# Performance work log

Hardware: AMD Instinct MI355X
Metric: run time of the kernel (lower is better)

Reference implementation:

```python
import jax, jax.numpy as jnp
import numpy as np

B = 65536      # batch
HID = 128      # hidden_dim
Q = 4          # IRK stages
DT = 0.1       # default time step
N_ITERS = 10   # fixed-point iterations


def setup_inputs() -> dict:
    key = jax.random.key(0)
    ks = jax.random.split(key, 16)
    def lin(k, fan_in, fan_out):
        return jax.random.normal(k, (fan_in, fan_out), jnp.float32) / np.sqrt(fan_in)
    return {
        "X0": jax.random.normal(ks[0], (B, 4), jnp.float32),
        "W1": lin(ks[1], 4, HID),   "b1": jnp.zeros((HID,), jnp.float32),
        "W2": lin(ks[2], HID, HID), "b2": jnp.zeros((HID,), jnp.float32),
        "W3": lin(ks[3], HID, HID), "b3": jnp.zeros((HID,), jnp.float32),
        "W4": lin(ks[4], HID, 4),   "b4": jnp.zeros((4,), jnp.float32),
        "lam1": jax.random.normal(ks[5], (1,), jnp.float32) * 0.1 + 0.5,
        "lam2": jax.random.normal(ks[6], (1,), jnp.float32) * 0.1 + 0.5,
        "lam3": jax.random.normal(ks[7], (1,), jnp.float32) * 0.1 + 0.5,
        "lam4": jax.random.normal(ks[8], (1,), jnp.float32) * 0.1 + 0.5,
        "IRK_alpha": jax.random.normal(ks[9], (Q, Q), jnp.float32) * 0.25,
        "IRK_beta": jax.random.normal(ks[10], (Q,), jnp.float32) * 0.25,
    }


def reference(X0, W1, b1, W2, b2, W3, b3, W4, b4,
              lam1, lam2, lam3, lam4, IRK_alpha, IRK_beta):
    dt = DT

    def mlp(x):  # (N,4) -> (N,4)
        h = jnp.tanh(x @ W1 + b1)
        h = jnp.tanh(h @ W2 + b2)
        h = jnp.tanh(h @ W3 + b3)
        return h @ W4 + b4

    def hamiltonian_vf(x):  # x: (N,4) = [p1,p2,q1,q2]
        H_out = mlp(x)
        dp_dt = -lam1 * H_out[:, 2:] - lam2 * x[:, 2:]
        dq_dt = lam3 * H_out[:, :2] + lam4 * x[:, :2]
        return jnp.concatenate([dp_dt, dq_dt], axis=1)

    bsz = X0.shape[0]
    K = jnp.zeros((bsz, Q, 4), X0.dtype)
    for _ in range(N_ITERS):  # small fixed trip count, unrolled
        # same contraction as original torch einsum 'bqi,ij->bqj'
        X_stages = X0[:, None, :] + dt * jnp.einsum('bqi,ij->bqj', K, IRK_alpha)
        K = hamiltonian_vf(X_stages.reshape(-1, 4)).reshape(bsz, Q, 4)

    # intended IRK final combine: X1 = X0 + dt * sum_q beta_q K[:,q,:]
    X1 = X0 + dt * jnp.einsum('bqi,q->bi', K, IRK_beta)
    return X1
```

## Files before the change

### kernel.cpp

```cpp
#include <hip/hip_runtime.h>
#include <hip/hip_bf16.h>
#include <stdint.h>

#define HID   128
#define DT    0.1f
#define NITER 10
#define RT    64
#define NT    256
#define HSTR  136

typedef __attribute__((ext_vector_type(8))) short bf16x8;
typedef __attribute__((ext_vector_type(4))) float f32x4;
typedef __attribute__((ext_vector_type(2))) unsigned int u32x2;
typedef __attribute__((ext_vector_type(4))) unsigned int u32x4;

struct alignas(16) Smem {
    uint16_t hA[RT * HSTR];
    uint16_t hB[RT * HSTR];
    uint16_t xb[RT * 8];
    uint32_t w4f[4 * 64 * 4];
    float    b1[HID], b2[HID], b3[HID];
    float    kk[RT * 4];
};

__device__ __forceinline__ uint16_t f2bf(float f) {
    uint32_t u = __float_as_uint(f);
    return (uint16_t)((u + 0x7fffu + ((u >> 16) & 1u)) >> 16);
}

__device__ __forceinline__ uint32_t pk2(float a, float b) {
    __hip_bfloat162 h = __float22bfloat162_rn(float2{a, b});
    return *reinterpret_cast<uint32_t*>(&h);
}

__device__ __forceinline__ float tanh_fast(float x) {
    float e = __builtin_amdgcn_exp2f(x * 2.885390081777927f);
    return fmaf(-2.0f, __builtin_amdgcn_rcpf(e + 1.0f), 1.0f);
}

__device__ __forceinline__ void dense_mfma(
    const bf16x8 (&wf)[2][4], const float* __restrict__ bias,
    const uint16_t* __restrict__ src, uint16_t* __restrict__ dst,
    int w, int ln, int g)
{
    f32x4 acc[2][4];
    #pragma unroll
    for (int mt = 0; mt < 2; ++mt) {
        f32x4 bs = *(const f32x4*)&bias[w * 32 + mt * 16 + 4 * g];
        #pragma unroll
        for (int nt = 0; nt < 4; ++nt) acc[mt][nt] = bs;
    }
    #pragma unroll
    for (int kt = 0; kt < 4; ++kt) {
        bf16x8 bfr[4];
        #pragma unroll
        for (int nt = 0; nt < 4; ++nt)
            bfr[nt] = *(const bf16x8*)&src[(nt * 16 + ln) * HSTR + kt * 32 + 8 * g];
        #pragma unroll
        for (int mt = 0; mt < 2; ++mt)
            #pragma unroll
            for (int nt = 0; nt < 4; ++nt)
                acc[mt][nt] = __builtin_amdgcn_mfma_f32_16x16x32_bf16(wf[mt][kt], bfr[nt], acc[mt][nt], 0, 0, 0);
    }
    #pragma unroll
    for (int mt = 0; mt < 2; ++mt) {
        int hb = w * 32 + mt * 16 + 4 * g;
        #pragma unroll
        for (int nt = 0; nt < 4; ++nt) {
            int r = nt * 16 + ln;
            u32x2 p;
            p.x = pk2(tanh_fast(acc[mt][nt][0]), tanh_fast(acc[mt][nt][1]));
            p.y = pk2(tanh_fast(acc[mt][nt][2]), tanh_fast(acc[mt][nt][3]));
            *(u32x2*)&dst[r * HSTR + hb] = p;
        }
    }
}

__global__ __launch_bounds__(NT, 3) void pinn_irk_mfma(
    const float* __restrict__ x0g,
    const float* __restrict__ w1g, const float* __restrict__ b1g,
    const float* __restrict__ w2g, const float* __restrict__ b2g,
    const float* __restrict__ w3g, const float* __restrict__ b3g,
    const float* __restrict__ w4g, const float* __restrict__ b4g,
    const float* __restrict__ l1g, const float* __restrict__ l2g,
    const float* __restrict__ l3g, const float* __restrict__ l4g,
    const float* __restrict__ alg, const float* __restrict__ beg,
    float* __restrict__ outg)
{
    __shared__ Smem S;
    const int t    = threadIdx.x;
    const int blk  = blockIdx.x;
    const int lane = t & 63;
    const int w    = t >> 6;
    const int ln   = lane & 15;
    const int g    = lane >> 4;
    const bool owner = (g == 0);
    const int r_own  = w * 16 + ln;

    const float L0 = l1g[0], L1v = l2g[0], L2v = l3g[0], L3v = l4g[0];
    const float B40 = b4g[0], B41 = b4g[1], B42 = b4g[2], B43 = b4g[3];

    if (t < HID) { S.b1[t] = b1g[t]; S.b2[t] = b2g[t]; S.b3[t] = b3g[t]; }
    {
        int r = t >> 2, c = 4 + (t & 3);
        S.xb[r * 8 + c] = 0;
    }
    {
        int kt = t >> 6, l = t & 63;
        int lns = l & 15, gs = l >> 4;
        uint32_t f[4];
        #pragma unroll
        for (int jj = 0; jj < 4; ++jj) {
            int k0 = kt * 32 + 8 * gs + 2 * jj;
            uint32_t lo = (lns < 4) ? (uint32_t)f2bf(w4g[k0 * 4 + lns]) : 0u;
            uint32_t hi = (lns < 4) ? (uint32_t)f2bf(w4g[(k0 + 1) * 4 + lns]) : 0u;
            f[jj] = lo | (hi << 16);
        }
        *(u32x4*)&S.w4f[t * 4] = (u32x4){f[0], f[1], f[2], f[3]};
    }

    float X0r[4] = {0.f, 0.f, 0.f, 0.f};
    float Xr[4]  = {0.f, 0.f, 0.f, 0.f};
    if (owner) {
        const float* xp = x0g + (blk * (RT / 4) + (r_own >> 2)) * 4;
        #pragma unroll
        for (int c = 0; c < 4; ++c) { X0r[c] = xp[c]; Xr[c] = X0r[c]; }
        u32x2 p;
        p.x = pk2(Xr[0], Xr[1]);
        p.y = pk2(Xr[2], Xr[3]);
        *(u32x2*)&S.xb[r_own * 8] = p;
    }

    bf16x8 w1f[2], w2f[2][4], w3f[2][4];
    {
        const int mcol = w * 32 + ln;
        #pragma unroll
        for (int mt = 0; mt < 2; ++mt) {
            bf16x8 f1;
            #pragma unroll
            for (int j = 0; j < 8; ++j) {
                int k = 8 * g + j;
                float v = (k < 4) ? w1g[k * HID + mcol + mt * 16] : 0.0f;
                f1[j] = (short)f2bf(v);
            }
            w1f[mt] = f1;
            #pragma unroll
            for (int kt = 0; kt < 4; ++kt) {
                bf16x8 f2, f3;
                #pragma unroll
                for (int j = 0; j < 8; ++j) {
                    int k = kt * 32 + 8 * g + j;
                    f2[j] = (short)f2bf(w2g[k * HID + mcol + mt * 16]);
                    f3[j] = (short)f2bf(w3g[k * HID + mcol + mt * 16]);
                }
                w2f[mt][kt] = f2;
                w3f[mt][kt] = f3;
            }
        }
    }
    __syncthreads();

    #pragma unroll 1
    for (int it = 0; it < NITER; ++it) {
        {
            f32x4 acc[2][4];
            #pragma unroll
            for (int mt = 0; mt < 2; ++mt) {
                f32x4 bs = *(const f32x4*)&S.b1[w * 32 + mt * 16 + 4 * g];
                #pragma unroll
                for (int nt = 0; nt < 4; ++nt) acc[mt][nt] = bs;
            }
            bf16x8 bfr[4];
            #pragma unroll
            for (int nt = 0; nt < 4; ++nt) bfr[nt] = (bf16x8){0,0,0,0,0,0,0,0};
            if (g == 0) {
                #pragma unroll
                for (int nt = 0; nt < 4; ++nt)
                    bfr[nt] = *(const bf16x8*)&S.xb[(nt * 16 + ln) * 8];
            }
            #pragma unroll
            for (int mt = 0; mt < 2; ++mt)
                #pragma unroll
                for (int nt = 0; nt < 4; ++nt)
                    acc[mt][nt] = __builtin_amdgcn_mfma_f32_16x16x32_bf16(w1f[mt], bfr[nt], acc[mt][nt], 0, 0, 0);
            #pragma unroll
            for (int mt = 0; mt < 2; ++mt) {
                int hb = w * 32 + mt * 16 + 4 * g;
                #pragma unroll
                for (int nt = 0; nt < 4; ++nt) {
                    int r = nt * 16 + ln;
                    u32x2 p;
                    p.x = pk2(tanh_fast(acc[mt][nt][0]), tanh_fast(acc[mt][nt][1]));
                    p.y = pk2(tanh_fast(acc[mt][nt][2]), tanh_fast(acc[mt][nt][3]));
                    *(u32x2*)&S.hA[r * HSTR + hb] = p;
                }
            }
        }
        __syncthreads();

        dense_mfma(w2f, S.b2, S.hA, S.hB, w, ln, g);
        __syncthreads();

        dense_mfma(w3f, S.b3, S.hB, S.hA, w, ln, g);
        __syncthreads();

        {
            f32x4 acc = (f32x4){0.f, 0.f, 0.f, 0.f};
            #pragma unroll
            for (int kt = 0; kt < 4; ++kt) {
                bf16x8 wfr = *(const bf16x8*)&S.w4f[(kt * 64 + lane) * 4];
                bf16x8 bfr = *(const bf16x8*)&S.hA[r_own * HSTR + kt * 32 + 8 * g];
                acc = __builtin_amdgcn_mfma_f32_16x16x32_bf16(wfr, bfr, acc, 0, 0, 0);
            }
            if (owner) {
                float h0 = acc[0] + B40, h1 = acc[1] + B41;
                float h2 = acc[2] + B42, h3 = acc[3] + B43;
                float kv0 = -L0 * h2 - L1v * Xr[2];
                float kv1 = -L0 * h3 - L1v * Xr[3];
                float kv2 =  L2v * h0 + L3v * Xr[0];
                float kv3 =  L2v * h1 + L3v * Xr[1];
                *(f32x4*)&S.kk[r_own * 4] = (f32x4){kv0, kv1, kv2, kv3};
                #pragma unroll
                for (int c = 0; c < 4; ++c) {
                    float s = kv0 * alg[c] + kv1 * alg[4 + c]
                            + kv2 * alg[8 + c] + kv3 * alg[12 + c];
                    Xr[c] = fmaf(DT, s, X0r[c]);
                }
                u32x2 p;
                p.x = pk2(Xr[0], Xr[1]);
                p.y = pk2(Xr[2], Xr[3]);
                *(u32x2*)&S.xb[r_own * 8] = p;
            }
        }
        __syncthreads();
    }

    if (t < RT) {
        int bb = t >> 2, i = t & 3;
        float s = beg[0] * S.kk[(bb * 4 + 0) * 4 + i]
                + beg[1] * S.kk[(bb * 4 + 1) * 4 + i]
                + beg[2] * S.kk[(bb * 4 + 2) * 4 + i]
                + beg[3] * S.kk[(bb * 4 + 3) * 4 + i];
        int bglob = blk * (RT / 4) + bb;
        outg[bglob * 4 + i] = x0g[bglob * 4 + i] + DT * s;
    }
}

extern "C" void kernel_launch(void* const* d_in, const int* in_sizes, int n_in,
                              void* d_out, int out_size, void* d_ws, size_t ws_size,
                              hipStream_t stream) {
    (void)in_sizes; (void)n_in; (void)d_ws; (void)ws_size; (void)out_size;

    const int n_rows = 65536 * 4;
    dim3 grid(n_rows / RT);
    dim3 block(NT);

    pinn_irk_mfma<<<grid, block, 0, stream>>>(
        (const float*)d_in[0],
        (const float*)d_in[1],  (const float*)d_in[2],
        (const float*)d_in[3],  (const float*)d_in[4],
        (const float*)d_in[5],  (const float*)d_in[6],
        (const float*)d_in[7],  (const float*)d_in[8],
        (const float*)d_in[9],  (const float*)d_in[10],
        (const float*)d_in[11], (const float*)d_in[12],
        (const float*)d_in[13], (const float*)d_in[14],
        (float*)d_out);
}
```

Before: 407.3 us.

## Use rational tanh approximation, keep biases in registers, alias kk into hB

Replaces the exp2+rcp tanh with a clamped Padé rational polynomial evaluated on float2 pairs, which removes the transcendental exp per element and permits packed FMA. Biases are now loaded into registers instead of shared memory, and the K output buffer reuses the hB region. LDS use drops, and launch bounds are raised from 3 to 4 blocks per CU to increase occupancy. The risks are register spills under the tighter bound and a less exact tanh near the clamp at ±3.5.

```diff
diff --git a/kernel.cpp b/kernel.cpp
--- a/kernel.cpp
+++ b/kernel.cpp
@@ -11,6 +11,7 @@
 
 typedef __attribute__((ext_vector_type(8))) short bf16x8;
 typedef __attribute__((ext_vector_type(4))) float f32x4;
+typedef __attribute__((ext_vector_type(2))) float f32x2;
 typedef __attribute__((ext_vector_type(2))) unsigned int u32x2;
 typedef __attribute__((ext_vector_type(4))) unsigned int u32x4;
 
@@ -19,8 +20,6 @@
     uint16_t hB[RT * HSTR];
     uint16_t xb[RT * 8];
     uint32_t w4f[4 * 64 * 4];
-    float    b1[HID], b2[HID], b3[HID];
-    float    kk[RT * 4];
 };
 
 __device__ __forceinline__ uint16_t f2bf(float f) {
@@ -33,23 +32,36 @@
     return *reinterpret_cast<uint32_t*>(&h);
 }
 
-__device__ __forceinline__ float tanh_fast(float x) {
-    float e = __builtin_amdgcn_exp2f(x * 2.885390081777927f);
-    return fmaf(-2.0f, __builtin_amdgcn_rcpf(e + 1.0f), 1.0f);
+__device__ __forceinline__ uint32_t tanh2_bf16(float a, float b) {
+    f32x2 x;
+    x.x = __builtin_amdgcn_fmed3f(a, -3.5f, 3.5f);
+    x.y = __builtin_amdgcn_fmed3f(b, -3.5f, 3.5f);
+    f32x2 s = x * x;
+    f32x2 n = s + 378.0f;
+    n = n * s + 17325.0f;
+    n = n * s + 135135.0f;
+    n = n * x;
+    f32x2 d = s * 28.0f + 3150.0f;
+    d = d * s + 62370.0f;
+    d = d * s + 135135.0f;
+    f32x2 r;
+    r.x = __builtin_amdgcn_rcpf(d.x);
+    r.y = __builtin_amdgcn_rcpf(d.y);
+    f32x2 res = n * r;
+    __hip_bfloat162 h = __float22bfloat162_rn(float2{res.x, res.y});
+    return *reinterpret_cast<uint32_t*>(&h);
 }
 
 __device__ __forceinline__ void dense_mfma(
-    const bf16x8 (&wf)[2][4], const float* __restrict__ bias,
+    const bf16x8 (&wf)[2][4], const f32x4 (&bs)[2],
     const uint16_t* __restrict__ src, uint16_t* __restrict__ dst,
     int w, int ln, int g)
 {
     f32x4 acc[2][4];
     #pragma unroll
-    for (int mt = 0; mt < 2; ++mt) {
-        f32x4 bs = *(const f32x4*)&bias[w * 32 + mt * 16 + 4 * g];
-        #pragma unroll
-        for (int nt = 0; nt < 4; ++nt) acc[mt][nt] = bs;
-    }
+    for (int mt = 0; mt < 2; ++mt)
+        #pragma unroll
+        for (int nt = 0; nt < 4; ++nt) acc[mt][nt] = bs[mt];
     #pragma unroll
     for (int kt = 0; kt < 4; ++kt) {
         bf16x8 bfr[4];
@@ -69,14 +81,14 @@
         for (int nt = 0; nt < 4; ++nt) {
             int r = nt * 16 + ln;
             u32x2 p;
-            p.x = pk2(tanh_fast(acc[mt][nt][0]), tanh_fast(acc[mt][nt][1]));
-            p.y = pk2(tanh_fast(acc[mt][nt][2]), tanh_fast(acc[mt][nt][3]));
+            p.x = tanh2_bf16(acc[mt][nt][0], acc[mt][nt][1]);
+            p.y = tanh2_bf16(acc[mt][nt][2], acc[mt][nt][3]);
             *(u32x2*)&dst[r * HSTR + hb] = p;
         }
     }
 }
 
-__global__ __launch_bounds__(NT, 3) void pinn_irk_mfma(
+__global__ __launch_bounds__(NT, 4) void pinn_irk_mfma(
     const float* __restrict__ x0g,
     const float* __restrict__ w1g, const float* __restrict__ b1g,
     const float* __restrict__ w2g, const float* __restrict__ b2g,
@@ -88,6 +100,7 @@
     float* __restrict__ outg)
 {
     __shared__ Smem S;
+    float* kkp = reinterpret_cast<float*>(S.hB);
     const int t    = threadIdx.x;
     const int blk  = blockIdx.x;
     const int lane = t & 63;
@@ -100,7 +113,15 @@
     const float L0 = l1g[0], L1v = l2g[0], L2v = l3g[0], L3v = l4g[0];
     const float B40 = b4g[0], B41 = b4g[1], B42 = b4g[2], B43 = b4g[3];
 
-    if (t < HID) { S.b1[t] = b1g[t]; S.b2[t] = b2g[t]; S.b3[t] = b3g[t]; }
+    f32x4 b1f[2], b2f[2], b3f[2];
+    #pragma unroll
+    for (int mt = 0; mt < 2; ++mt) {
+        int hb = w * 32 + mt * 16 + 4 * g;
+        b1f[mt] = *(const f32x4*)&b1g[hb];
+        b2f[mt] = *(const f32x4*)&b2g[hb];
+        b3f[mt] = *(const f32x4*)&b3g[hb];
+    }
+
     {
         int r = t >> 2, c = 4 + (t & 3);
         S.xb[r * 8 + c] = 0;
@@ -165,11 +186,9 @@
         {
             f32x4 acc[2][4];
             #pragma unroll
-            for (int mt = 0; mt < 2; ++mt) {
-                f32x4 bs = *(const f32x4*)&S.b1[w * 32 + mt * 16 + 4 * g];
-                #pragma unroll
-                for (int nt = 0; nt < 4; ++nt) acc[mt][nt] = bs;
-            }
+            for (int mt = 0; mt < 2; ++mt)
+                #pragma unroll
+                for (int nt = 0; nt < 4; ++nt) acc[mt][nt] = b1f[mt];
             bf16x8 bfr[4];
             #pragma unroll
             for (int nt = 0; nt < 4; ++nt) bfr[nt] = (bf16x8){0,0,0,0,0,0,0,0};
@@ -190,18 +209,18 @@
                 for (int nt = 0; nt < 4; ++nt) {
                     int r = nt * 16 + ln;
                     u32x2 p;
-                    p.x = pk2(tanh_fast(acc[mt][nt][0]), tanh_fast(acc[mt][nt][1]));
-                    p.y = pk2(tanh_fast(acc[mt][nt][2]), tanh_fast(acc[mt][nt][3]));
+                    p.x = tanh2_bf16(acc[mt][nt][0], acc[mt][nt][1]);
+                    p.y = tanh2_bf16(acc[mt][nt][2], acc[mt][nt][3]);
                     *(u32x2*)&S.hA[r * HSTR + hb] = p;
                 }
             }
         }
         __syncthreads();
 
-        dense_mfma(w2f, S.b2, S.hA, S.hB, w, ln, g);
-        __syncthreads();
-
-        dense_mfma(w3f, S.b3, S.hB, S.hA, w, ln, g);
+        dense_mfma(w2f, b2f, S.hA, S.hB, w, ln, g);
+        __syncthreads();
+
+        dense_mfma(w3f, b3f, S.hB, S.hA, w, ln, g);
         __syncthreads();
 
         {
@@ -219,7 +238,7 @@
                 float kv1 = -L0 * h3 - L1v * Xr[3];
                 float kv2 =  L2v * h0 + L3v * Xr[0];
                 float kv3 =  L2v * h1 + L3v * Xr[1];
-                *(f32x4*)&S.kk[r_own * 4] = (f32x4){kv0, kv1, kv2, kv3};
+                *(f32x4*)&kkp[r_own * 4] = (f32x4){kv0, kv1, kv2, kv3};
                 #pragma unroll
                 for (int c = 0; c < 4; ++c) {
                     float s = kv0 * alg[c] + kv1 * alg[4 + c]
@@ -237,10 +256,10 @@
 
     if (t < RT) {
         int bb = t >> 2, i = t & 3;
-        float s = beg[0] * S.kk[(bb * 4 + 0) * 4 + i]
-                + beg[1] * S.kk[(bb * 4 + 1) * 4 + i]
-                + beg[2] * S.kk[(bb * 4 + 2) * 4 + i]
-                + beg[3] * S.kk[(bb * 4 + 3) * 4 + i];
+        float s = beg[0] * kkp[(bb * 4 + 0) * 4 + i]
+                + beg[1] * kkp[(bb * 4 + 1) * 4 + i]
+                + beg[2] * kkp[(bb * 4 + 2) * 4 + i]
+                + beg[3] * kkp[(bb * 4 + 3) * 4 + i];
         int bglob = blk * (RT / 4) + bb;
         outg[bglob * 4 + i] = x0g[bglob * 4 + i] + DT * s;
     }
```

Measured after the change: 536.0 us. +31.6%, slower.
